# Kernel optimization log

Hardware: AMD Instinct MI355X
Metric: run time of the kernel (lower is better)

The kernel has to match this reference:

```python
import math
import jax, jax.numpy as jnp
import numpy as np

T, D, H = 2048, 2048, 16
C = D // H
EPS = 1e-6


def _rope_tables(c, t):
    inv_freq = 1.0 / (10000.0 ** (jnp.arange(0, c, 2, dtype=jnp.float32) / c))
    freqs = jnp.arange(t, dtype=jnp.float32)[:, None] * inv_freq[None, :]  # (T, C/2)
    return jnp.sin(freqs), jnp.cos(freqs)


def _rotate_every_two(x):
    x1 = x[..., ::2]
    x2 = x[..., 1::2]
    return jnp.stack((-x2, x1), axis=-1).reshape(x.shape)


def _apply_rope(x_htc, sin, cos):
    # sin/cos: (T, C/2) -> repeat each freq twice along channel -> (1, T, C)
    sin = jnp.repeat(sin, 2, axis=-1)[None]
    cos = jnp.repeat(cos, 2, axis=-1)[None]
    return x_htc * cos + _rotate_every_two(x_htc) * sin


def _layernorm(x, w):
    mu = jnp.mean(x, axis=-1, keepdims=True)
    var = jnp.var(x, axis=-1, keepdims=True)
    return (x - mu) / jnp.sqrt(var + EPS) * w


def setup_inputs() -> dict:
    key = jax.random.key(0)
    ks = jax.random.split(key, 4)
    x = jax.random.normal(ks[0], (T, D), dtype=jnp.float32)
    W_attn = jax.random.normal(ks[1], (3 * D, D), dtype=jnp.float32) * 0.02
    b_attn = jnp.zeros((3 * D,), dtype=jnp.float32)
    W_proj = jax.random.normal(ks[2], (D, D), dtype=jnp.float32) * 0.02
    b_proj = jnp.zeros((D,), dtype=jnp.float32)
    q_ln_w = jnp.ones((C,), dtype=jnp.float32)
    k_ln_w = jnp.ones((C,), dtype=jnp.float32)
    return {"x": x, "W_attn": W_attn, "b_attn": b_attn, "W_proj": W_proj,
            "b_proj": b_proj, "q_ln_w": q_ln_w, "k_ln_w": k_ln_w}


def reference(x, W_attn, b_attn, W_proj, b_proj, q_ln_w, k_ln_w):
    t, d = x.shape
    qkv = x @ W_attn.T + b_attn                      # (T, 3D)
    q, k, v = jnp.split(qkv, 3, axis=-1)
    q = q.reshape(t, H, C).transpose(1, 0, 2)        # (H, T, C)
    k = k.reshape(t, H, C).transpose(1, 0, 2)
    v = v.reshape(t, H, C).transpose(1, 0, 2)
    q = _layernorm(q, q_ln_w)
    k = _layernorm(k, k_ln_w)
    sin, cos = _rope_tables(C, t)
    q = _apply_rope(q, sin, cos)
    k = _apply_rope(k, sin, cos)
    a = jnp.einsum("htc,hsc->hts", q, k)             # (H, T, T)
    causal = jnp.tril(jnp.ones((1, t, t))) == 0
    a = jnp.where(causal, float("-inf"), a)
    scaling = math.sqrt(C)                            # q_ln active
    a = jax.nn.softmax(a.astype(jnp.float32) / scaling, axis=-1).astype(x.dtype)
    out = jnp.einsum("hts,hsc->htc", a, v)           # (H, T, C)
    out = out.transpose(1, 0, 2).reshape(t, d)       # (T, D)
    return out @ W_proj.T + b_proj
```

## Files before the change

kernel.cpp:

```cpp
#include <hip/hip_runtime.h>
#include <hip/hip_bf16.h>
#include <math.h>

#define T_DIM 2048
#define D_DIM 2048
#define H_DIM 16
#define C_DIM 128

typedef __bf16 bf16;
typedef __attribute__((ext_vector_type(8))) __bf16 bf16x8;
typedef __attribute__((ext_vector_type(4))) __bf16 bf16x4;
typedef __attribute__((ext_vector_type(2))) __bf16 bf16x2;
typedef __attribute__((ext_vector_type(4))) float f32x4;

__device__ __forceinline__ void gload_lds16(const void* g, void* l) {
  __builtin_amdgcn_global_load_lds((__attribute__((address_space(1))) void*)g,
                                   (__attribute__((address_space(3))) void*)l,
                                   16, 0, 0);
}

__global__ __launch_bounds__(256) void cvt3(
    const float* __restrict__ x, const float* __restrict__ wa, const float* __restrict__ wp,
    bf16* __restrict__ xo, bf16* __restrict__ wao, bf16* __restrict__ wpo)
{
  const int NX = 1048576, NA = 3145728;
  int i = blockIdx.x * 256 + threadIdx.x;
  for (; i < 5242880; i += 2048 * 256) {
    const float* s; bf16* d; int off;
    if (i < NX)            { s = x;  d = xo;  off = i; }
    else if (i < NX + NA)  { s = wa; d = wao; off = i - NX; }
    else                   { s = wp; d = wpo; off = i - NX - NA; }
    float4 v = reinterpret_cast<const float4*>(s)[off];
    bf16x4 o;
    o[0] = (bf16)v.x; o[1] = (bf16)v.y; o[2] = (bf16)v.z; o[3] = (bf16)v.w;
    reinterpret_cast<bf16x4*>(d)[off] = o;
  }
}

template <typename OutT>
__global__ __launch_bounds__(512, 2) void gemm384_bt_bias(
    const bf16* __restrict__ A, const bf16* __restrict__ B,
    const float* __restrict__ bias, OutT* __restrict__ C,
    int M, int N, int K)
{
  __shared__ __align__(16) bf16 Asl[2][128 * 64];
  __shared__ __align__(16) bf16 Bsl[2][384 * 64];
  const int tid = threadIdx.x;
  const int lane = tid & 63;
  const int wv = tid >> 6;
  const int g = lane >> 4, r16 = lane & 15;
  const int wm = wv >> 2;
  const int wn = wv & 3;

  int bid = blockIdx.x;
  int bid2 = (bid & 7) * (gridDim.x >> 3) + (bid >> 3);
  const int ntn = N / 384;
  const int bn = bid2 % ntn, bm = bid2 / ntn;

  const size_t Abase = (size_t)(bm * 128) * K;
  const size_t Bbase = (size_t)(bn * 384) * K;

  f32x4 acc[2][2][2][3] = {};
  bf16x8 a0[2][2], a1[2][2];
  bf16x8 b0[3][2], b1[3][2];

  auto stageA = [&](int bb, int t) {
#pragma unroll
    for (int i = 0; i < 2; ++i) {
      int c = i * 512 + tid;
      int r = c >> 3, p = c & 7, j = p ^ (r & 7);
      gload_lds16(A + Abase + (size_t)r * K + t * 64 + j * 8,
                  (char*)&Asl[bb][0] + (size_t)c * 16);
    }
  };
  auto stageB = [&](int bb, int u, int t) {
#pragma unroll
    for (int i = 0; i < 2; ++i) {
      int c = i * 512 + tid;
      int r = c >> 3, p = c & 7, j = p ^ (r & 7);
      gload_lds16(B + Bbase + (size_t)(u * 128 + r) * K + t * 64 + j * 8,
                  (char*)&Bsl[bb][0] + u * 16384 + (size_t)c * 16);
    }
  };
  auto readAh = [&](bf16x8 (&dst)[2][2], int bufi, int qr) {
#pragma unroll
    for (int R = 0; R < 2; ++R) {
      int ar = wm * 64 + qr * 32 + R * 16 + r16;
#pragma unroll
      for (int ks = 0; ks < 2; ++ks)
        dst[R][ks] = *reinterpret_cast<const bf16x8*>(
            &Asl[bufi][ar * 64 + (((ks * 4 + g) ^ (ar & 7)) << 3)]);
    }
  };
  auto readBh = [&](bf16x8 (&dst)[3][2], int bufi, int qc) {
#pragma unroll
    for (int F = 0; F < 3; ++F) {
      int br = wn * 96 + qc * 48 + F * 16 + r16;
#pragma unroll
      for (int ks = 0; ks < 2; ++ks)
        dst[F][ks] = *reinterpret_cast<const bf16x8*>(
            &Bsl[bufi][br * 64 + (((ks * 4 + g) ^ (br & 7)) << 3)]);
    }
  };
  auto mfma12 = [&](f32x4 (&cq)[2][3], bf16x8 (&aa)[2][2], bf16x8 (&bb)[3][2]) {
#pragma unroll
    for (int ks = 0; ks < 2; ++ks)
#pragma unroll
      for (int R = 0; R < 2; ++R)
#pragma unroll
        for (int F = 0; F < 3; ++F)
          cq[R][F] = __builtin_amdgcn_mfma_f32_16x16x32_bf16(aa[R][ks], bb[F][ks], cq[R][F], 0, 0, 0);
  };

  stageA(0, 0); stageB(0, 0, 0); stageB(0, 1, 0); stageB(0, 2, 0);
  __syncthreads();

  const int NT = K >> 6;
  for (int t = 0; t < NT; ++t) {
    const int cb = t & 1, nb = cb ^ 1;
    if (t + 1 < NT) {
      stageA(nb, t + 1); stageB(nb, 0, t + 1); stageB(nb, 1, t + 1); stageB(nb, 2, t + 1);
    }
    readAh(a0, cb, 0); readAh(a1, cb, 1);
    readBh(b0, cb, 0); readBh(b1, cb, 1);
    mfma12(acc[0][0], a0, b0);
    mfma12(acc[0][1], a0, b1);
    mfma12(acc[1][1], a1, b1);
    mfma12(acc[1][0], a1, b0);
    __syncthreads();
  }

#pragma unroll
  for (int qr = 0; qr < 2; ++qr)
#pragma unroll
    for (int qc = 0; qc < 2; ++qc)
#pragma unroll
      for (int R = 0; R < 2; ++R)
#pragma unroll
        for (int F = 0; F < 3; ++F) {
          int row0 = bm * 128 + wm * 64 + qr * 32 + R * 16 + g * 4;
          int col  = bn * 384 + wn * 96 + qc * 48 + F * 16 + r16;
          float bv = bias[col];
#pragma unroll
          for (int rr = 0; rr < 4; ++rr)
            C[(size_t)(row0 + rr) * N + col] = (OutT)(acc[qr][qc][R][F][rr] + bv);
        }
}

__global__ __launch_bounds__(256, 2) void gemm_bt_bias(
    const bf16* __restrict__ A, const bf16* __restrict__ B,
    const float* __restrict__ bias, float* __restrict__ C,
    int M, int N, int K)
{
  __shared__ __align__(16) bf16 As[2][128 * 64];
  __shared__ __align__(16) bf16 Bs[2][128 * 64];
  const int tid = threadIdx.x;
  const int lane = tid & 63;
  const int w = tid >> 6;
  const int wm = (w >> 1) * 64, wn = (w & 1) * 64;
  const int g = lane >> 4;
  const int r16 = lane & 15;

  int lb = blockIdx.y * gridDim.x + blockIdx.x;
  int nblk = gridDim.x * gridDim.y;
  int s = (lb & 7) * (nblk >> 3) + (lb >> 3);
  const int bn = s % gridDim.x, bm = s / gridDim.x;

  f32x4 acc[4][4] = {};

  const size_t Abase = (size_t)(bm * 128) * K;
  const size_t Bbase = (size_t)(bn * 128) * K;

  auto stage = [&](int bb, int t) {
#pragma unroll
    for (int i = 0; i < 4; ++i) {
      int c = i * 256 + tid;
      int r = c >> 3, p = c & 7, j = p ^ (r & 7);
      gload_lds16(A + Abase + (size_t)r * K + t * 64 + j * 8,
                  (char*)&As[bb][0] + (size_t)c * 16);
      gload_lds16(B + Bbase + (size_t)r * K + t * 64 + j * 8,
                  (char*)&Bs[bb][0] + (size_t)c * 16);
    }
  };

  stage(0, 0);
  __syncthreads();

  const int NT = K >> 6;
  for (int t = 0; t < NT; ++t) {
    const int cb = t & 1, nb = cb ^ 1;
    if (t + 1 < NT) stage(nb, t + 1);
    bf16x8 a[4][2], b[4][2];
#pragma unroll
    for (int m = 0; m < 4; ++m) {
      int ar = wm + m * 16 + r16;
#pragma unroll
      for (int ks = 0; ks < 2; ++ks)
        a[m][ks] = *reinterpret_cast<const bf16x8*>(
            &As[cb][ar * 64 + (((ks * 4 + g) ^ (ar & 7)) << 3)]);
    }
#pragma unroll
    for (int n = 0; n < 4; ++n) {
      int br = wn + n * 16 + r16;
#pragma unroll
      for (int ks = 0; ks < 2; ++ks)
        b[n][ks] = *reinterpret_cast<const bf16x8*>(
            &Bs[cb][br * 64 + (((ks * 4 + g) ^ (br & 7)) << 3)]);
    }
#pragma unroll
    for (int ks = 0; ks < 2; ++ks)
#pragma unroll
      for (int m = 0; m < 4; ++m)
#pragma unroll
        for (int n = 0; n < 4; ++n)
          acc[m][n] = __builtin_amdgcn_mfma_f32_16x16x32_bf16(a[m][ks], b[n][ks], acc[m][n], 0, 0, 0);
    __syncthreads();
  }

#pragma unroll
  for (int m = 0; m < 4; ++m) {
    int row0 = bm * 128 + wm + m * 16 + g * 4;
#pragma unroll
    for (int n = 0; n < 4; ++n) {
      int col = bn * 128 + wn + n * 16 + r16;
      float bv = bias[col];
#pragma unroll
      for (int rr = 0; rr < 4; ++rr)
        C[(size_t)(row0 + rr) * N + col] = acc[m][n][rr] + bv;
    }
  }
}

__global__ __launch_bounds__(256) void lnrope_vt_kernel(
    const bf16* __restrict__ qkv, const float* __restrict__ qw,
    const float* __restrict__ kw, bf16* __restrict__ qo, bf16* __restrict__ ko,
    bf16* __restrict__ vt)
{
  __shared__ bf16 tile[32][36];
  const int tid = threadIdx.x;
  if (blockIdx.x < 4096) {
    const int lane = tid & 63;
    const int wid = blockIdx.x * 4 + (tid >> 6);
    const int rid = wid * 2 + (lane >> 5);
    const int h = rid >> 11;
    const int t = rid & (T_DIM - 1);
    const int c0 = (lane & 31) * 4;

    float if0 = exp2f(-13.287712379549449f * (float)c0 * (1.0f / 128.0f));
    float if1 = exp2f(-13.287712379549449f * (float)(c0 + 2) * (1.0f / 128.0f));
    float fr0 = (float)t * if0, fr1 = (float)t * if1;
    float sn0 = sinf(fr0), cs0 = cosf(fr0);
    float sn1 = sinf(fr1), cs1 = cosf(fr1);
    const float scaleq = 0.08838834764831845f;

#pragma unroll
    for (int which = 0; which < 2; ++which) {
      const bf16* base = qkv + (size_t)t * (3 * D_DIM) + which * D_DIM + h * C_DIM + c0;
      bf16x4 v4 = *reinterpret_cast<const bf16x4*>(base);
      float x0 = (float)v4[0], x1 = (float)v4[1], x2 = (float)v4[2], x3 = (float)v4[3];
      float s = x0 + x1 + x2 + x3;
#pragma unroll
      for (int m = 16; m; m >>= 1) s += __shfl_xor(s, m);
      float mu = s * (1.0f / 128.0f);
      float d0 = x0 - mu, d1 = x1 - mu, d2 = x2 - mu, d3 = x3 - mu;
      float ss = d0 * d0 + d1 * d1 + d2 * d2 + d3 * d3;
#pragma unroll
      for (int m = 16; m; m >>= 1) ss += __shfl_xor(ss, m);
      float rstd = rsqrtf(ss * (1.0f / 128.0f) + 1e-6f);
      const float* wgt = which ? kw : qw;
      float4 wv = *reinterpret_cast<const float4*>(wgt + c0);
      float y0 = d0 * rstd * wv.x, y1 = d1 * rstd * wv.y;
      float y2 = d2 * rstd * wv.z, y3 = d3 * rstd * wv.w;
      float o0 = y0 * cs0 - y1 * sn0;
      float o1 = y1 * cs0 + y0 * sn0;
      float o2 = y2 * cs1 - y3 * sn1;
      float o3 = y3 * cs1 + y2 * sn1;
      if (!which) { o0 *= scaleq; o1 *= scaleq; o2 *= scaleq; o3 *= scaleq; }
      bf16x4 ob; ob[0] = (bf16)o0; ob[1] = (bf16)o1; ob[2] = (bf16)o2; ob[3] = (bf16)o3;
      *reinterpret_cast<bf16x4*>(
          (which ? ko : qo) + ((size_t)h * T_DIM + t) * C_DIM + c0) = ob;
    }
  } else {
    const int vb = blockIdx.x - 4096;
    const int t0 = (vb & 63) * 32;
    const int c0 = ((vb >> 6) & 3) * 32;
    const int h = vb >> 8;
    {
      int row = tid >> 3, col4 = (tid & 7) * 4;
      *reinterpret_cast<bf16x4*>(&tile[row][col4]) =
          *reinterpret_cast<const bf16x4*>(
              &qkv[(size_t)(t0 + row) * (3 * D_DIM) + 2 * D_DIM + h * C_DIM + c0 + col4]);
    }
    __syncthreads();
    {
      int c = tid >> 3, t4 = (tid & 7) * 4;
      bf16x4 ob;
      ob[0] = tile[t4][c];     ob[1] = tile[t4 + 1][c];
      ob[2] = tile[t4 + 2][c]; ob[3] = tile[t4 + 3][c];
      *reinterpret_cast<bf16x4*>(
          &vt[((size_t)h * C_DIM + c0 + c) * T_DIM + t0 + t4]) = ob;
    }
  }
}

__global__ __launch_bounds__(256, 4) void attn_kernel(
    const bf16* __restrict__ Q, const bf16* __restrict__ K,
    const bf16* __restrict__ VT, bf16* __restrict__ AO,
    float* __restrict__ U, float* __restrict__ ML)
{
  __shared__ __align__(16) bf16 Ks[2][32 * 128];
  __shared__ __align__(16) bf16 Vs[2][128 * 32];
  __shared__ __align__(16) bf16 p_lds[4][16 * 32];
  const int tid = threadIdx.x;
  const int lane = tid & 63;
  const int w = tid >> 6;
  const int g = lane >> 4, r16 = lane & 15;
  const int h = blockIdx.y;
  const int b = blockIdx.x;

  int qb, kb0, kb1, sp;
  if (b < 32) { qb = 16 + (b >> 1); sp = b & 1; kb0 = sp * 32; kb1 = sp ? (2 * qb + 2) : 32; }
  else        { qb = 47 - b;        sp = -1;    kb0 = 0;       kb1 = 2 * qb + 2; }
  const int qr0 = qb * 64 + w * 16;
  const int qrow = qr0 + r16;

  const bf16* Qh = Q + (size_t)h * T_DIM * C_DIM;
  const bf16* Kh = K + (size_t)h * T_DIM * C_DIM;
  const bf16* Vh = VT + (size_t)h * C_DIM * T_DIM;

  bf16x8 qf[4];
#pragma unroll
  for (int kk = 0; kk < 4; ++kk)
    qf[kk] = *reinterpret_cast<const bf16x8*>(
        &Qh[(size_t)qrow * C_DIM + kk * 32 + g * 8]);

  float mrow = -INFINITY, lrow = 0.f;
  f32x4 o[8] = {};

  auto stage = [&](int bb, int kb) {
    const bf16* Kt = Kh + (size_t)(kb * 32) * C_DIM;
    const bf16* Vt = Vh + kb * 32;
#pragma unroll
    for (int i = 0; i < 2; ++i) {
      int e = i * 256 + tid;
      int r = e >> 4, p = e & 15, j = p ^ (r & 7);
      gload_lds16(Kt + r * C_DIM + j * 8, (char*)&Ks[bb][0] + (size_t)e * 16);
    }
#pragma unroll
    for (int i = 0; i < 2; ++i) {
      int e = i * 256 + tid;
      int r = e >> 2, p = e & 3, j = p ^ ((r >> 1) & 3);
      gload_lds16(Vt + (size_t)r * T_DIM + j * 8, (char*)&Vs[bb][0] + (size_t)e * 16);
    }
  };

  stage(0, kb0);
  __syncthreads();
  int buf = 0;

  for (int kb = kb0; kb < kb1; ++kb) {
    if (kb + 1 < kb1) stage(buf ^ 1, kb + 1);

    f32x4 sacc[2] = {};
    __builtin_amdgcn_s_setprio(1);
#pragma unroll
    for (int n = 0; n < 2; ++n) {
      int kr = n * 16 + r16;
      const bf16* kbase = &Ks[buf][kr << 7];
#pragma unroll
      for (int kk = 0; kk < 4; ++kk) {
        bf16x8 kf = *reinterpret_cast<const bf16x8*>(
            kbase + (((kk * 4 + g) ^ (kr & 7)) << 3));
        sacc[n] = __builtin_amdgcn_mfma_f32_16x16x32_bf16(kf, qf[kk], sacc[n], 0, 0, 0);
      }
    }
    __builtin_amdgcn_s_setprio(0);
    if (kb * 32 + 31 > qr0) {
#pragma unroll
      for (int n = 0; n < 2; ++n)
#pragma unroll
        for (int rr = 0; rr < 4; ++rr)
          if (kb * 32 + n * 16 + g * 4 + rr > qrow) sacc[n][rr] = -3.0e38f;
    }
    float mx = fmaxf(fmaxf(fmaxf(sacc[0][0], sacc[0][1]), fmaxf(sacc[0][2], sacc[0][3])),
                     fmaxf(fmaxf(sacc[1][0], sacc[1][1]), fmaxf(sacc[1][2], sacc[1][3])));
    mx = fmaxf(mx, __shfl_xor(mx, 16));
    mx = fmaxf(mx, __shfl_xor(mx, 32));
    float alpha = 1.0f;
    bool need = __any(mx > mrow + 8.0f);
    if (need) {
      float mnew = fmaxf(mrow, mx);
      alpha = __expf(mrow - mnew);
      mrow = mnew;
    }
    float ps = 0.f;
#pragma unroll
    for (int n = 0; n < 2; ++n)
#pragma unroll
      for (int rr = 0; rr < 4; ++rr) {
        float p = __expf(sacc[n][rr] - mrow);
        sacc[n][rr] = p;
        ps += p;
      }
    ps += __shfl_xor(ps, 16);
    ps += __shfl_xor(ps, 32);
    lrow = lrow * alpha + ps;
    if (need) {
#pragma unroll
      for (int nc = 0; nc < 8; ++nc)
#pragma unroll
        for (int rr = 0; rr < 4; ++rr)
          o[nc][rr] *= alpha;
    }
    {
      bf16* prow = &p_lds[w][r16 << 5];
      const int ssw = (r16 >> 1) & 3;
#pragma unroll
      for (int n = 0; n < 2; ++n) {
        bf16x4 pk;
        pk[0] = (bf16)sacc[n][0]; pk[1] = (bf16)sacc[n][1];
        pk[2] = (bf16)sacc[n][2]; pk[3] = (bf16)sacc[n][3];
        int c8 = 2 * n + (g >> 1);
        *reinterpret_cast<bf16x4*>(prow + (((c8 ^ ssw) << 3) | ((g & 1) << 2))) = pk;
      }
    }
    asm volatile("s_waitcnt lgkmcnt(0)" ::: "memory");
    __builtin_amdgcn_s_setprio(1);
    bf16x8 pf = *reinterpret_cast<const bf16x8*>(
        &p_lds[w][(r16 << 5) + ((g ^ ((r16 >> 1) & 3)) << 3)]);
#pragma unroll
    for (int nc = 0; nc < 8; ++nc) {
      int vr = nc * 16 + r16;
      bf16x8 vf = *reinterpret_cast<const bf16x8*>(
          &Vs[buf][(vr << 5) + ((g ^ ((vr >> 1) & 3)) << 3)]);
      o[nc] = __builtin_amdgcn_mfma_f32_16x16x32_bf16(vf, pf, o[nc], 0, 0, 0);
    }
    __builtin_amdgcn_s_setprio(0);
    __syncthreads();
    buf ^= 1;
  }

  if (sp < 0) {
    float inv = 1.0f / lrow;
    bf16* arow = &AO[(size_t)qrow * D_DIM + h * C_DIM + (g << 2)];
#pragma unroll
    for (int nc = 0; nc < 8; ++nc) {
      bf16x4 ob;
      ob[0] = (bf16)(o[nc][0] * inv); ob[1] = (bf16)(o[nc][1] * inv);
      ob[2] = (bf16)(o[nc][2] * inv); ob[3] = (bf16)(o[nc][3] * inv);
      *reinterpret_cast<bf16x4*>(arow + nc * 16) = ob;
    }
  } else {
    const int qi = qb - 16;
    const size_t ubase = ((size_t)(h * 16 + qi) * 2 + sp) * (64 * 128);
    const size_t mlbase = (size_t)(h * 16 + qi) * 256 + sp * 128;
    const int row = w * 16 + r16;
    float* urow = &U[ubase + (size_t)row * 128 + (g << 2)];
#pragma unroll
    for (int nc = 0; nc < 8; ++nc)
      *reinterpret_cast<f32x4*>(urow + nc * 16) = o[nc];
    if (g == 0) {
      ML[mlbase + row] = mrow;
      ML[mlbase + 64 + row] = lrow;
    }
  }
}

__global__ __launch_bounds__(256) void attn_combine(
    const float* __restrict__ U, const float* __restrict__ ML, bf16* __restrict__ AO)
{
  int idx = blockIdx.x * 256 + threadIdx.x;
  int c4 = (idx & 31) * 4;
  int r = idx >> 5;
  int trow = r & 63;
  int qi = (r >> 6) & 15;
  int h = r >> 10;

  size_t mlbase = (size_t)(h * 16 + qi) * 256;
  float m0 = ML[mlbase + trow],       l0 = ML[mlbase + 64 + trow];
  float m1 = ML[mlbase + 128 + trow], l1 = ML[mlbase + 192 + trow];
  float m = fmaxf(m0, m1);
  float a0 = __expf(m0 - m), a1 = __expf(m1 - m);
  float inv = 1.0f / (l0 * a0 + l1 * a1);

  size_t t0 = ((size_t)(h * 16 + qi) * 2) * (64 * 128) + (size_t)trow * 128 + c4;
  float4 u0 = *reinterpret_cast<const float4*>(U + t0);
  float4 u1 = *reinterpret_cast<const float4*>(U + t0 + 64 * 128);
  int t = 1024 + qi * 64 + trow;
  bf16x4 ob;
  ob[0] = (bf16)((u0.x * a0 + u1.x * a1) * inv);
  ob[1] = (bf16)((u0.y * a0 + u1.y * a1) * inv);
  ob[2] = (bf16)((u0.z * a0 + u1.z * a1) * inv);
  ob[3] = (bf16)((u0.w * a0 + u1.w * a1) * inv);
  *reinterpret_cast<bf16x4*>(&AO[(size_t)t * D_DIM + h * C_DIM + c4]) = ob;
}

extern "C" void kernel_launch(void* const* d_in, const int* in_sizes, int n_in,
                              void* d_out, int out_size, void* d_ws, size_t ws_size,
                              hipStream_t stream)
{
  const float* x      = (const float*)d_in[0];
  const float* W_attn = (const float*)d_in[1];
  const float* b_attn = (const float*)d_in[2];
  const float* W_proj = (const float*)d_in[3];
  const float* b_proj = (const float*)d_in[4];
  const float* q_ln_w = (const float*)d_in[5];
  const float* k_ln_w = (const float*)d_in[6];

  char* ws = (char*)d_ws;
  bf16*  x_bf  = (bf16*)(ws + 0);
  bf16*  wa_bf = (bf16*)(ws + 8388608);
  bf16*  wp_bf = (bf16*)(ws + 33554432);
  bf16*  qkv   = (bf16*)(ws + 41943040);
  float* U     = (float*)(ws + 67108864);
  float* ML    = (float*)(ws + 83886080);
  bf16*  q_bf  = (bf16*)(ws + 92274688);
  bf16*  k_bf  = (bf16*)(ws + 100663296);
  bf16*  vt    = (bf16*)(ws + 109051904);
  bf16*  ao    = (bf16*)(ws + 117440512);

  cvt3<<<2048, 256, 0, stream>>>(x, W_attn, W_proj, x_bf, wa_bf, wp_bf);

  gemm384_bt_bias<bf16><<<dim3((T_DIM / 128) * (3 * D_DIM / 384)), dim3(512), 0, stream>>>(
      x_bf, wa_bf, b_attn, qkv, T_DIM, 3 * D_DIM, D_DIM);

  lnrope_vt_kernel<<<4096 + 4096, 256, 0, stream>>>(qkv, q_ln_w, k_ln_w, q_bf, k_bf, vt);

  attn_kernel<<<dim3(48, H_DIM), 256, 0, stream>>>(q_bf, k_bf, vt, ao, U, ML);
  attn_combine<<<2048, 256, 0, stream>>>(U, ML, ao);

  gemm_bt_bias<<<dim3(D_DIM / 128, T_DIM / 128), 256, 0, stream>>>(
      ao, wp_bf, b_proj, (float*)d_out, T_DIM, D_DIM, D_DIM);
}
```

Before: 168.0 us.

## Split causal attention into many KV segments with single-buffered LDS and bf16 partials

Replaces the old 48-block-per-head scheme, where only the later query blocks were split in two, with 144 blocks per head. The first four query blocks run unsplit, and each later group of four gets progressively more KV segments (2, 3, ...), balancing work and raising the block count. LDS is reduced to a single K/V buffer and launch bounds are raised to 8 blocks per CU for occupancy, at the cost of losing the prefetch/compute overlap. Partial outputs are stored in bf16 and reuse the dead qkv workspace. The combine kernel now merges a variable number of segments, which costs some precision in the partial sums.

New measurement: 348.7 us. 2.08x slower.

```diff
diff --git a/kernel.cpp b/kernel.cpp
--- a/kernel.cpp
+++ b/kernel.cpp
@@ -303,13 +303,13 @@
   }
 }
 
-__global__ __launch_bounds__(256, 4) void attn_kernel(
+__global__ __launch_bounds__(256, 8) void attn_kernel(
     const bf16* __restrict__ Q, const bf16* __restrict__ K,
     const bf16* __restrict__ VT, bf16* __restrict__ AO,
-    float* __restrict__ U, float* __restrict__ ML)
-{
-  __shared__ __align__(16) bf16 Ks[2][32 * 128];
-  __shared__ __align__(16) bf16 Vs[2][128 * 32];
+    bf16* __restrict__ U, float* __restrict__ ML)
+{
+  __shared__ __align__(16) bf16 Ks[32 * 128];
+  __shared__ __align__(16) bf16 Vs[128 * 32];
   __shared__ __align__(16) bf16 p_lds[4][16 * 32];
   const int tid = threadIdx.x;
   const int lane = tid & 63;
@@ -318,9 +318,20 @@
   const int h = blockIdx.y;
   const int b = blockIdx.x;
 
-  int qb, kb0, kb1, sp;
-  if (b < 32) { qb = 16 + (b >> 1); sp = b & 1; kb0 = sp * 32; kb1 = sp ? (2 * qb + 2) : 32; }
-  else        { qb = 47 - b;        sp = -1;    kb0 = 0;       kb1 = 2 * qb + 2; }
+  int qb, sp, nseg;
+  if (b < 4) { qb = b; sp = -1; nseg = 1; }
+  else {
+    int gg = 0, cum = 4;
+    while (b >= cum + 4 * (gg + 2)) { cum += 4 * (gg + 2); ++gg; }
+    int off = b - cum;
+    nseg = gg + 2;
+    qb = 4 + 4 * gg + off / nseg;
+    sp = off % nseg;
+  }
+  const int ntile = 2 * qb + 2;
+  const int kb0 = (sp < 0) ? 0 : (ntile * sp) / nseg;
+  const int kb1 = (sp < 0) ? ntile : (ntile * (sp + 1)) / nseg;
+
   const int qr0 = qb * 64 + w * 16;
   const int qrow = qr0 + r16;
 
@@ -337,36 +348,36 @@
   float mrow = -INFINITY, lrow = 0.f;
   f32x4 o[8] = {};
 
-  auto stage = [&](int bb, int kb) {
+  auto stage = [&](int kb) {
     const bf16* Kt = Kh + (size_t)(kb * 32) * C_DIM;
     const bf16* Vt = Vh + kb * 32;
 #pragma unroll
     for (int i = 0; i < 2; ++i) {
       int e = i * 256 + tid;
       int r = e >> 4, p = e & 15, j = p ^ (r & 7);
-      gload_lds16(Kt + r * C_DIM + j * 8, (char*)&Ks[bb][0] + (size_t)e * 16);
+      gload_lds16(Kt + r * C_DIM + j * 8, (char*)&Ks[0] + (size_t)e * 16);
     }
 #pragma unroll
     for (int i = 0; i < 2; ++i) {
       int e = i * 256 + tid;
       int r = e >> 2, p = e & 3, j = p ^ ((r >> 1) & 3);
-      gload_lds16(Vt + (size_t)r * T_DIM + j * 8, (char*)&Vs[bb][0] + (size_t)e * 16);
-    }
-  };
-
-  stage(0, kb0);
-  __syncthreads();
-  int buf = 0;
+      gload_lds16(Vt + (size_t)r * T_DIM + j * 8, (char*)&Vs[0] + (size_t)e * 16);
+    }
+  };
+
+  stage(kb0);
 
   for (int kb = kb0; kb < kb1; ++kb) {
-    if (kb + 1 < kb1) stage(buf ^ 1, kb + 1);
+    asm volatile("s_waitcnt vmcnt(0)" ::: "memory");
+    __builtin_amdgcn_s_barrier();
+    __builtin_amdgcn_sched_barrier(0);
 
     f32x4 sacc[2] = {};
     __builtin_amdgcn_s_setprio(1);
 #pragma unroll
     for (int n = 0; n < 2; ++n) {
       int kr = n * 16 + r16;
-      const bf16* kbase = &Ks[buf][kr << 7];
+      const bf16* kbase = &Ks[kr << 7];
 #pragma unroll
       for (int kk = 0; kk < 4; ++kk) {
         bf16x8 kf = *reinterpret_cast<const bf16x8*>(
@@ -432,12 +443,12 @@
     for (int nc = 0; nc < 8; ++nc) {
       int vr = nc * 16 + r16;
       bf16x8 vf = *reinterpret_cast<const bf16x8*>(
-          &Vs[buf][(vr << 5) + ((g ^ ((vr >> 1) & 3)) << 3)]);
+          &Vs[(vr << 5) + ((g ^ ((vr >> 1) & 3)) << 3)]);
       o[nc] = __builtin_amdgcn_mfma_f32_16x16x32_bf16(vf, pf, o[nc], 0, 0, 0);
     }
     __builtin_amdgcn_s_setprio(0);
     __syncthreads();
-    buf ^= 1;
+    if (kb + 1 < kb1) stage(kb + 1);
   }
 
   if (sp < 0) {
@@ -451,47 +462,58 @@
       *reinterpret_cast<bf16x4*>(arow + nc * 16) = ob;
     }
   } else {
-    const int qi = qb - 16;
-    const size_t ubase = ((size_t)(h * 16 + qi) * 2 + sp) * (64 * 128);
-    const size_t mlbase = (size_t)(h * 16 + qi) * 256 + sp * 128;
+    const int slot = h * 140 + (b - 4);
+    const size_t ubase = (size_t)slot * (64 * 128);
+    const size_t mlb = (size_t)slot * 128;
     const int row = w * 16 + r16;
-    float* urow = &U[ubase + (size_t)row * 128 + (g << 2)];
-#pragma unroll
-    for (int nc = 0; nc < 8; ++nc)
-      *reinterpret_cast<f32x4*>(urow + nc * 16) = o[nc];
+    bf16* urow = &U[ubase + (size_t)row * 128 + (g << 2)];
+#pragma unroll
+    for (int nc = 0; nc < 8; ++nc) {
+      bf16x4 ub;
+      ub[0] = (bf16)o[nc][0]; ub[1] = (bf16)o[nc][1];
+      ub[2] = (bf16)o[nc][2]; ub[3] = (bf16)o[nc][3];
+      *reinterpret_cast<bf16x4*>(urow + nc * 16) = ub;
+    }
     if (g == 0) {
-      ML[mlbase + row] = mrow;
-      ML[mlbase + 64 + row] = lrow;
+      ML[mlb + row] = mrow;
+      ML[mlb + 64 + row] = lrow;
     }
   }
 }
 
 __global__ __launch_bounds__(256) void attn_combine(
-    const float* __restrict__ U, const float* __restrict__ ML, bf16* __restrict__ AO)
+    const bf16* __restrict__ U, const float* __restrict__ ML, bf16* __restrict__ AO)
 {
   int idx = blockIdx.x * 256 + threadIdx.x;
   int c4 = (idx & 31) * 4;
   int r = idx >> 5;
   int trow = r & 63;
-  int qi = (r >> 6) & 15;
-  int h = r >> 10;
-
-  size_t mlbase = (size_t)(h * 16 + qi) * 256;
-  float m0 = ML[mlbase + trow],       l0 = ML[mlbase + 64 + trow];
-  float m1 = ML[mlbase + 128 + trow], l1 = ML[mlbase + 192 + trow];
-  float m = fmaxf(m0, m1);
-  float a0 = __expf(m0 - m), a1 = __expf(m1 - m);
-  float inv = 1.0f / (l0 * a0 + l1 * a1);
-
-  size_t t0 = ((size_t)(h * 16 + qi) * 2) * (64 * 128) + (size_t)trow * 128 + c4;
-  float4 u0 = *reinterpret_cast<const float4*>(U + t0);
-  float4 u1 = *reinterpret_cast<const float4*>(U + t0 + 64 * 128);
-  int t = 1024 + qi * 64 + trow;
+  int hq = r >> 6;
+  int qi = hq % 28;
+  int h = hq / 28;
+  int g = qi >> 2;
+  int nseg = g + 2;
+  int slot0 = h * 140 + (2 * g * g + 6 * g) + (qi - 4 * g) * nseg;
+
+  float m = -INFINITY;
+  for (int s = 0; s < nseg; ++s)
+    m = fmaxf(m, ML[(size_t)(slot0 + s) * 128 + trow]);
+  float L = 0.f;
+  float ox = 0.f, oy = 0.f, oz = 0.f, ow = 0.f;
+  for (int s = 0; s < nseg; ++s) {
+    size_t mlb = (size_t)(slot0 + s) * 128;
+    float a = __expf(ML[mlb + trow] - m);
+    L += ML[mlb + 64 + trow] * a;
+    bf16x4 u = *reinterpret_cast<const bf16x4*>(
+        U + (size_t)(slot0 + s) * (64 * 128) + (size_t)trow * 128 + c4);
+    ox += (float)u[0] * a; oy += (float)u[1] * a;
+    oz += (float)u[2] * a; ow += (float)u[3] * a;
+  }
+  float inv = 1.0f / L;
+  int t = (qi + 4) * 64 + trow;
   bf16x4 ob;
-  ob[0] = (bf16)((u0.x * a0 + u1.x * a1) * inv);
-  ob[1] = (bf16)((u0.y * a0 + u1.y * a1) * inv);
-  ob[2] = (bf16)((u0.z * a0 + u1.z * a1) * inv);
-  ob[3] = (bf16)((u0.w * a0 + u1.w * a1) * inv);
+  ob[0] = (bf16)(ox * inv); ob[1] = (bf16)(oy * inv);
+  ob[2] = (bf16)(oz * inv); ob[3] = (bf16)(ow * inv);
   *reinterpret_cast<bf16x4*>(&AO[(size_t)t * D_DIM + h * C_DIM + c4]) = ob;
 }
 
@@ -512,12 +534,12 @@
   bf16*  wa_bf = (bf16*)(ws + 8388608);
   bf16*  wp_bf = (bf16*)(ws + 33554432);
   bf16*  qkv   = (bf16*)(ws + 41943040);
-  float* U     = (float*)(ws + 67108864);
-  float* ML    = (float*)(ws + 83886080);
   bf16*  q_bf  = (bf16*)(ws + 92274688);
   bf16*  k_bf  = (bf16*)(ws + 100663296);
   bf16*  vt    = (bf16*)(ws + 109051904);
   bf16*  ao    = (bf16*)(ws + 117440512);
+  bf16*  U  = (bf16*)(ws + 41943040);
+  float* ML = (float*)(ws + 78643200);
 
   cvt3<<<2048, 256, 0, stream>>>(x, W_attn, W_proj, x_bf, wa_bf, wp_bf);
 
@@ -526,8 +548,8 @@
 
   lnrope_vt_kernel<<<4096 + 4096, 256, 0, stream>>>(qkv, q_ln_w, k_ln_w, q_bf, k_bf, vt);
 
-  attn_kernel<<<dim3(48, H_DIM), 256, 0, stream>>>(q_bf, k_bf, vt, ao, U, ML);
-  attn_combine<<<2048, 256, 0, stream>>>(U, ML, ao);
+  attn_kernel<<<dim3(144, H_DIM), 256, 0, stream>>>(q_bf, k_bf, vt, ao, U, ML);
+  attn_combine<<<3584, 256, 0, stream>>>(U, ML, ao);
 
   gemm_bt_bias<<<dim3(D_DIM / 128, T_DIM / 128), 256, 0, stream>>>(
       ao, wp_bf, b_proj, (float*)d_out, T_DIM, D_DIM, D_DIM);
```

## Use four-stage LDS pipeline with K=32 tiles and explicit vmcnt waits in GEMMs

Applied to the files above, without the earlier changes.

Both GEMM kernels move from a double-buffered K=64 loop to a four-buffer ring of K=32 stages, issuing loads three tiles ahead. Explicit s_waitcnt vmcnt values plus a single s_barrier per iteration replace the trailing __syncthreads. This is meant to hide global-load latency better with the same LDS footprint. The cost is more loop iterations and barriers, and correctness depends on the hand-set vmcnt counts matching the number of loads issued per stage.

Measured after the change: 198.2 us. +18.0%, slower.

```diff
diff --git a/kernel.cpp b/kernel.cpp
--- a/kernel.cpp
+++ b/kernel.cpp
@@ -43,8 +43,8 @@
     const float* __restrict__ bias, OutT* __restrict__ C,
     int M, int N, int K)
 {
-  __shared__ __align__(16) bf16 Asl[2][128 * 64];
-  __shared__ __align__(16) bf16 Bsl[2][384 * 64];
+  __shared__ __align__(16) bf16 Asl[4][64 * 64];
+  __shared__ __align__(16) bf16 Bsl[4][3 * 64 * 64];
   const int tid = threadIdx.x;
   const int lane = tid & 63;
   const int wv = tid >> 6;
@@ -61,73 +61,69 @@
   const size_t Bbase = (size_t)(bn * 384) * K;
 
   f32x4 acc[2][2][2][3] = {};
-  bf16x8 a0[2][2], a1[2][2];
-  bf16x8 b0[3][2], b1[3][2];
-
-  auto stageA = [&](int bb, int t) {
-#pragma unroll
-    for (int i = 0; i < 2; ++i) {
-      int c = i * 512 + tid;
-      int r = c >> 3, p = c & 7, j = p ^ (r & 7);
-      gload_lds16(A + Abase + (size_t)r * K + t * 64 + j * 8,
+
+  auto stage = [&](int bb, int t) {
+    {
+      int c = tid;
+      int lr = c >> 3, cp = c & 7, j = cp ^ (lr & 7);
+      int r = lr + ((j >> 2) << 6);
+      gload_lds16(A + Abase + (size_t)r * K + t * 32 + (j & 3) * 8,
                   (char*)&Asl[bb][0] + (size_t)c * 16);
     }
+#pragma unroll
+    for (int u = 0; u < 3; ++u) {
+      int c = tid;
+      int lr = c >> 3, cp = c & 7, j = cp ^ (lr & 7);
+      int r = lr + ((j >> 2) << 6);
+      gload_lds16(B + Bbase + (size_t)(u * 128 + r) * K + t * 32 + (j & 3) * 8,
+                  (char*)&Bsl[bb][0] + u * 8192 + (size_t)c * 16);
+    }
   };
-  auto stageB = [&](int bb, int u, int t) {
-#pragma unroll
-    for (int i = 0; i < 2; ++i) {
-      int c = i * 512 + tid;
-      int r = c >> 3, p = c & 7, j = p ^ (r & 7);
-      gload_lds16(B + Bbase + (size_t)(u * 128 + r) * K + t * 64 + j * 8,
-                  (char*)&Bsl[bb][0] + u * 16384 + (size_t)c * 16);
-    }
-  };
-  auto readAh = [&](bf16x8 (&dst)[2][2], int bufi, int qr) {
+  auto readA = [&](bf16x8 (&dst)[2], int bb, int qr) {
 #pragma unroll
     for (int R = 0; R < 2; ++R) {
       int ar = wm * 64 + qr * 32 + R * 16 + r16;
-#pragma unroll
-      for (int ks = 0; ks < 2; ++ks)
-        dst[R][ks] = *reinterpret_cast<const bf16x8*>(
-            &Asl[bufi][ar * 64 + (((ks * 4 + g) ^ (ar & 7)) << 3)]);
+      int lr = ar & 63, cpos = ((ar >> 6) << 2) + g;
+      dst[R] = *reinterpret_cast<const bf16x8*>(
+          &Asl[bb][lr * 64 + ((cpos ^ (lr & 7)) << 3)]);
     }
   };
-  auto readBh = [&](bf16x8 (&dst)[3][2], int bufi, int qc) {
+  auto readB = [&](bf16x8 (&dst)[3], int bb, int qc) {
 #pragma unroll
     for (int F = 0; F < 3; ++F) {
       int br = wn * 96 + qc * 48 + F * 16 + r16;
-#pragma unroll
-      for (int ks = 0; ks < 2; ++ks)
-        dst[F][ks] = *reinterpret_cast<const bf16x8*>(
-            &Bsl[bufi][br * 64 + (((ks * 4 + g) ^ (br & 7)) << 3)]);
+      int u = br >> 7, wr = br & 127;
+      int lr = wr & 63, cpos = ((wr >> 6) << 2) + g;
+      dst[F] = *reinterpret_cast<const bf16x8*>(
+          &Bsl[bb][u * 4096 + lr * 64 + ((cpos ^ (lr & 7)) << 3)]);
     }
   };
-  auto mfma12 = [&](f32x4 (&cq)[2][3], bf16x8 (&aa)[2][2], bf16x8 (&bb)[3][2]) {
-#pragma unroll
-    for (int ks = 0; ks < 2; ++ks)
-#pragma unroll
-      for (int R = 0; R < 2; ++R)
-#pragma unroll
-        for (int F = 0; F < 3; ++F)
-          cq[R][F] = __builtin_amdgcn_mfma_f32_16x16x32_bf16(aa[R][ks], bb[F][ks], cq[R][F], 0, 0, 0);
-  };
-
-  stageA(0, 0); stageB(0, 0, 0); stageB(0, 1, 0); stageB(0, 2, 0);
-  __syncthreads();
-
-  const int NT = K >> 6;
+
+  stage(0, 0); stage(1, 1); stage(2, 2);
+
+  const int NT = K >> 5;
   for (int t = 0; t < NT; ++t) {
-    const int cb = t & 1, nb = cb ^ 1;
-    if (t + 1 < NT) {
-      stageA(nb, t + 1); stageB(nb, 0, t + 1); stageB(nb, 1, t + 1); stageB(nb, 2, t + 1);
-    }
-    readAh(a0, cb, 0); readAh(a1, cb, 1);
-    readBh(b0, cb, 0); readBh(b1, cb, 1);
-    mfma12(acc[0][0], a0, b0);
-    mfma12(acc[0][1], a0, b1);
-    mfma12(acc[1][1], a1, b1);
-    mfma12(acc[1][0], a1, b0);
-    __syncthreads();
+    const int rem = NT - 1 - t;
+    if (rem >= 2)      { asm volatile("s_waitcnt vmcnt(8)" ::: "memory"); }
+    else if (rem == 1) { asm volatile("s_waitcnt vmcnt(4)" ::: "memory"); }
+    else               { asm volatile("s_waitcnt vmcnt(0)" ::: "memory"); }
+    __builtin_amdgcn_s_barrier();
+    __builtin_amdgcn_sched_barrier(0);
+    if (t + 3 < NT) stage((t + 3) & 3, t + 3);
+
+    const int cb = t & 3;
+    bf16x8 a0[2], a1[2], b0[3], b1[3];
+    readA(a0, cb, 0); readA(a1, cb, 1);
+    readB(b0, cb, 0); readB(b1, cb, 1);
+#pragma unroll
+    for (int R = 0; R < 2; ++R)
+#pragma unroll
+      for (int F = 0; F < 3; ++F) {
+        acc[0][0][R][F] = __builtin_amdgcn_mfma_f32_16x16x32_bf16(a0[R], b0[F], acc[0][0][R][F], 0, 0, 0);
+        acc[0][1][R][F] = __builtin_amdgcn_mfma_f32_16x16x32_bf16(a0[R], b1[F], acc[0][1][R][F], 0, 0, 0);
+        acc[1][1][R][F] = __builtin_amdgcn_mfma_f32_16x16x32_bf16(a1[R], b1[F], acc[1][1][R][F], 0, 0, 0);
+        acc[1][0][R][F] = __builtin_amdgcn_mfma_f32_16x16x32_bf16(a1[R], b0[F], acc[1][0][R][F], 0, 0, 0);
+      }
   }
 
 #pragma unroll
@@ -152,8 +148,8 @@
     const float* __restrict__ bias, float* __restrict__ C,
     int M, int N, int K)
 {
-  __shared__ __align__(16) bf16 As[2][128 * 64];
-  __shared__ __align__(16) bf16 Bs[2][128 * 64];
+  __shared__ __align__(16) bf16 As[4][64 * 64];
+  __shared__ __align__(16) bf16 Bs[4][64 * 64];
   const int tid = threadIdx.x;
   const int lane = tid & 63;
   const int w = tid >> 6;
@@ -173,48 +169,50 @@
 
   auto stage = [&](int bb, int t) {
 #pragma unroll
-    for (int i = 0; i < 4; ++i) {
+    for (int i = 0; i < 2; ++i) {
       int c = i * 256 + tid;
-      int r = c >> 3, p = c & 7, j = p ^ (r & 7);
-      gload_lds16(A + Abase + (size_t)r * K + t * 64 + j * 8,
+      int lr = c >> 3, cp = c & 7, j = cp ^ (lr & 7);
+      int r = lr + ((j >> 2) << 6);
+      gload_lds16(A + Abase + (size_t)r * K + t * 32 + (j & 3) * 8,
                   (char*)&As[bb][0] + (size_t)c * 16);
-      gload_lds16(B + Bbase + (size_t)r * K + t * 64 + j * 8,
+      gload_lds16(B + Bbase + (size_t)r * K + t * 32 + (j & 3) * 8,
                   (char*)&Bs[bb][0] + (size_t)c * 16);
     }
   };
 
-  stage(0, 0);
-  __syncthreads();
-
-  const int NT = K >> 6;
+  stage(0, 0); stage(1, 1); stage(2, 2);
+
+  const int NT = K >> 5;
   for (int t = 0; t < NT; ++t) {
-    const int cb = t & 1, nb = cb ^ 1;
-    if (t + 1 < NT) stage(nb, t + 1);
-    bf16x8 a[4][2], b[4][2];
+    const int rem = NT - 1 - t;
+    if (rem >= 2)      { asm volatile("s_waitcnt vmcnt(8)" ::: "memory"); }
+    else if (rem == 1) { asm volatile("s_waitcnt vmcnt(4)" ::: "memory"); }
+    else               { asm volatile("s_waitcnt vmcnt(0)" ::: "memory"); }
+    __builtin_amdgcn_s_barrier();
+    __builtin_amdgcn_sched_barrier(0);
+    if (t + 3 < NT) stage((t + 3) & 3, t + 3);
+
+    const int cb = t & 3;
+    bf16x8 a[4], b[4];
 #pragma unroll
     for (int m = 0; m < 4; ++m) {
       int ar = wm + m * 16 + r16;
-#pragma unroll
-      for (int ks = 0; ks < 2; ++ks)
-        a[m][ks] = *reinterpret_cast<const bf16x8*>(
-            &As[cb][ar * 64 + (((ks * 4 + g) ^ (ar & 7)) << 3)]);
+      int lr = ar & 63, cpos = ((ar >> 6) << 2) + g;
+      a[m] = *reinterpret_cast<const bf16x8*>(
+          &As[cb][lr * 64 + ((cpos ^ (lr & 7)) << 3)]);
     }
 #pragma unroll
     for (int n = 0; n < 4; ++n) {
       int br = wn + n * 16 + r16;
-#pragma unroll
-      for (int ks = 0; ks < 2; ++ks)
-        b[n][ks] = *reinterpret_cast<const bf16x8*>(
-            &Bs[cb][br * 64 + (((ks * 4 + g) ^ (br & 7)) << 3)]);
-    }
-#pragma unroll
-    for (int ks = 0; ks < 2; ++ks)
-#pragma unroll
-      for (int m = 0; m < 4; ++m)
-#pragma unroll
-        for (int n = 0; n < 4; ++n)
-          acc[m][n] = __builtin_amdgcn_mfma_f32_16x16x32_bf16(a[m][ks], b[n][ks], acc[m][n], 0, 0, 0);
-    __syncthreads();
+      int lr = br & 63, cpos = ((br >> 6) << 2) + g;
+      b[n] = *reinterpret_cast<const bf16x8*>(
+          &Bs[cb][lr * 64 + ((cpos ^ (lr & 7)) << 3)]);
+    }
+#pragma unroll
+    for (int m = 0; m < 4; ++m)
+#pragma unroll
+      for (int n = 0; n < 4; ++n)
+        acc[m][n] = __builtin_amdgcn_mfma_f32_16x16x32_bf16(a[m], b[n], acc[m][n], 0, 0, 0);
   }
 
 #pragma unroll
```
